# Kernel optimization log

Measured on AMD Instinct MI355X. Metric: run time of the kernel, lower is better.

## Reference

```python
import jax, jax.numpy as jnp
import numpy as np

T, B = 32, 512          # frames, batch
HALF = 42               # rows per hand (21 landmarks x 2 coords)
HF = 300                # per-hand feature size
HID = 500               # hidden size
OUT = 10                # output classes
DN = ('NCH', 'OIH', 'NCH')


def setup_inputs() -> dict:
    key = jax.random.key(0)
    ks = jax.random.split(key, 18)
    n = lambda k, s: jax.random.normal(k, s, dtype=jnp.float32) * 0.05
    return dict(
        hand_data=jax.random.normal(ks[0], (T, B, 2 * HALF), dtype=jnp.float32),
        hidden=jnp.zeros((B, HID), jnp.float32),
        l_conv_w=n(ks[1], (16, 2, 2)), l_conv_b=n(ks[2], (16,)),
        l_fc_w=n(ks[3], (HF, 304)),    l_fc_b=n(ks[4], (HF,)),
        r_conv_w=n(ks[5], (16, 2, 2)), r_conv_b=n(ks[6], (16,)),
        r_fc_w=n(ks[7], (HF, 304)),    r_fc_b=n(ks[8], (HF,)),
        conv2_w=n(ks[9], (32, 2, 2)),  conv2_b=n(ks[10], (32,)),
        l2_w=n(ks[11], (HID, 9504)),   l2_b=n(ks[12], (HID,)),
        h2h_w=n(ks[13], (HID, HID)),   h2h_b=n(ks[14], (HID,)),
        out_w=n(ks[15], (OUT, HID)),   out_b=n(ks[16], (OUT,)),
    )


def _maxpool1d(y, k):
    return jax.lax.reduce_window(y, -jnp.inf, jax.lax.max,
                                 (1, 1, k), (1, 1, 1), 'VALID')


def _hand(x, cw, cb, fw, fb):
    # x: (N, 2, 21) -> conv k2 -> (N,16,20) -> relu -> pool k2 -> (N,16,19)
    y = jax.lax.conv_general_dilated(x, cw, (1,), 'VALID', dimension_numbers=DN)
    y = jax.nn.relu(y + cb[None, :, None])
    y = _maxpool1d(y, 2)
    y = y.reshape(y.shape[0], -1)          # (N, 304)
    return jax.nn.relu(y @ fw.T + fb)      # (N, 300)


def reference(hand_data, hidden,
              l_conv_w, l_conv_b, l_fc_w, l_fc_b,
              r_conv_w, r_conv_b, r_fc_w, r_fc_b,
              conv2_w, conv2_b, l2_w, l2_b,
              h2h_w, h2h_b, out_w, out_b):
    t, b, r = hand_data.shape
    half = r // 2
    # (T,B,42) -> (T*B,21,2) -> (T*B,2,21); per-frame branches have no
    # recurrence, so we vectorize them over all frames at once.
    left = jnp.swapaxes(hand_data[:, :, :half].reshape(t * b, -1, 2), 1, 2)
    right = jnp.swapaxes(hand_data[:, :, half:].reshape(t * b, -1, 2), 1, 2)
    lo = _hand(left, l_conv_w, l_conv_b, l_fc_w, l_fc_b)    # (T*B, 300)
    ro = _hand(right, r_conv_w, r_conv_b, r_fc_w, r_fc_b)   # (T*B, 300)
    both = jnp.stack([lo, ro], axis=1)                       # (T*B, 2, 300)
    y = jax.lax.conv_general_dilated(both, conv2_w, (1,), 'VALID',
                                     dimension_numbers=DN)   # (T*B, 32, 299)
    y = jax.nn.relu(y + conv2_b[None, :, None])
    y = _maxpool1d(y, 3)                                     # (T*B, 32, 297)
    y = y.reshape(t * b, -1)                                 # (T*B, 9504)
    i2h = (y @ l2_w.T + l2_b).reshape(t, b, -1)              # (T, B, 500)

    def step(h, i2h_t):
        h = h @ h2h_w.T + h2h_b                              # hidden = h2h(hidden)
        out = jax.nn.relu((i2h_t + h) @ out_w.T + out_b)
        return h, out

    hidden, outs = jax.lax.scan(step, hidden, i2h)
    return outs[-1], hidden
```

## Files before the change

### kernel.cpp

```cpp
#include <hip/hip_runtime.h>
#include <hip/hip_bf16.h>


typedef __attribute__((ext_vector_type(8))) unsigned short us8;
typedef __attribute__((ext_vector_type(8))) __bf16 bf8v;
typedef __attribute__((ext_vector_type(4))) float f4v;

static __device__ __forceinline__ unsigned short f2bf(float x) {
    __hip_bfloat16 h = __float2bfloat16(x);
    return *reinterpret_cast<unsigned short*>(&h);
}

static __device__ __forceinline__ void gload16(const void* g, void* s) {
    typedef __attribute__((address_space(1))) const void gv_t;
    typedef __attribute__((address_space(3))) void sv_t;
    __builtin_amdgcn_global_load_lds((gv_t*)g, (sv_t*)s, 16, 0, 0);
}

static __device__ __forceinline__ float4 ldg4_guard(
    const float* __restrict__ p, int r, int R, int c, int C, int ld)
{
    float4 v = make_float4(0.f, 0.f, 0.f, 0.f);
    if (r < R) {
        if (c + 3 < C) {
            v = *(const float4*)(p + (size_t)r * ld + c);
        } else {
            float tmp[4] = {0.f, 0.f, 0.f, 0.f};
            for (int u = 0; u < 4; ++u)
                if (c + u < C) tmp[u] = p[(size_t)r * ld + c + u];
            v = make_float4(tmp[0], tmp[1], tmp[2], tmp[3]);
        }
    }
    return v;
}

#define KSTR 9536

__global__ __launch_bounds__(256, 2) void mfma_bt(
    const unsigned short* __restrict__ A, const unsigned short* __restrict__ B,
    float* __restrict__ Cp, int nper, int ntot)
{
    __shared__ alignas(16) unsigned short Al[2][4096];
    __shared__ alignas(16) unsigned short Bl[2][4096];
    const int lid = blockIdx.x;
    const int z = lid & 7;
    const int bm = ((lid >> 3) & 7) * 64, bn = (lid >> 6) * 64;
    int s0 = z * nper;
    int s1 = s0 + nper; if (s1 > ntot) s1 = ntot;
    const int ns = s1 - s0;
    const int t = threadIdx.x, w = t >> 6, l = t & 63;
    const int srow = l >> 3;
    const int sslot = (l & 7) ^ srow;
    const int wm = (w >> 1) * 32, wn = (w & 1) * 32;
    const int fr = l & 15, jj = l >> 4;
    f4v acc[2][2] = {};

    const unsigned short* Ab = A + (size_t)(bm + 16 * w + srow) * KSTR + sslot * 8;
    const unsigned short* Bb = B + (size_t)(bn + 16 * w + srow) * KSTR + sslot * 8;

#define STAGE(buf, st)                                                          \
    {                                                                           \
        size_t k0 = (size_t)(s0 + (st)) * 64;                                   \
        _Pragma("unroll")                                                       \
        for (int q = 0; q < 2; ++q) {                                           \
            gload16(Ab + (size_t)(8 * q) * KSTR + k0,                           \
                    &Al[buf][(16 * w + 8 * q) * 64]);                           \
            gload16(Bb + (size_t)(8 * q) * KSTR + k0,                           \
                    &Bl[buf][(16 * w + 8 * q) * 64]);                           \
        }                                                                       \
    }

#define COMPUTE(buf)                                                            \
    {                                                                           \
        _Pragma("unroll")                                                       \
        for (int kk = 0; kk < 2; ++kk) {                                        \
            bf8v af[2], bf[2];                                                  \
            _Pragma("unroll")                                                   \
            for (int f = 0; f < 2; ++f) {                                       \
                int rA = wm + f * 16 + fr;                                      \
                int pA = (jj + 4 * kk) ^ (rA & 7);                              \
                af[f] = __builtin_bit_cast(bf8v,                                \
                        *(const us8*)&Al[buf][rA * 64 + pA * 8]);               \
                int rB = wn + f * 16 + fr;                                      \
                int pB = (jj + 4 * kk) ^ (rB & 7);                              \
                bf[f] = __builtin_bit_cast(bf8v,                                \
                        *(const us8*)&Bl[buf][rB * 64 + pB * 8]);               \
            }                                                                   \
            _Pragma("unroll")                                                   \
            for (int fi = 0; fi < 2; ++fi)                                      \
                _Pragma("unroll")                                               \
                for (int fj = 0; fj < 2; ++fj)                                  \
                    acc[fi][fj] = __builtin_amdgcn_mfma_f32_16x16x32_bf16(      \
                        af[fi], bf[fj], acc[fi][fj], 0, 0, 0);                  \
        }                                                                       \
    }

    STAGE(0, 0);
    __syncthreads();
    int cur = 0;
    for (int st = 0; st < ns; ++st) {
        if (st + 1 < ns) STAGE(cur ^ 1, st + 1);
        COMPUTE(cur);
        __syncthreads();
        cur ^= 1;
    }

    float* Cz = Cp + (size_t)z * 262144;
#pragma unroll
    for (int fi = 0; fi < 2; ++fi)
#pragma unroll
        for (int fj = 0; fj < 2; ++fj)
#pragma unroll
            for (int r = 0; r < 4; ++r) {
                int m = bm + wm + fi * 16 + jj * 4 + r;
                int n = bn + wn + fj * 16 + fr;
                Cz[(size_t)m * 512 + n] = acc[fi][fj][r];
            }
#undef STAGE
#undef COMPUTE
}


__global__ __launch_bounds__(256) void fc_gemm(
    const float* __restrict__ hpL, const float* __restrict__ hpR,
    const float* __restrict__ lfw, const float* __restrict__ rfw,
    const float* __restrict__ lfb, const float* __restrict__ rfb,
    float* __restrict__ both)
{
    __shared__ alignas(16) float As[16][68];
    __shared__ alignas(16) float Bs[16][68];
    const int hand = blockIdx.z;
    const float* A = hand ? hpR : hpL;
    const float* B = hand ? rfw : lfw;
    const float* bias = hand ? rfb : lfb;
    const int t = threadIdx.x;
    const int bm = blockIdx.x * 64, bn = blockIdx.y * 64;
    const int lr = t >> 2, kq = (t & 3) * 4;
    const int ty = t >> 4, tx = t & 15;
    float acc[4][4] = {};
    float4 a0 = *(const float4*)(A + (size_t)(bm + lr) * 304 + kq);
    float4 b0 = (bn + lr < 300)
        ? *(const float4*)(B + (size_t)(bn + lr) * 304 + kq)
        : make_float4(0.f, 0.f, 0.f, 0.f);
    for (int ks = 0; ks < 19; ++ks) {
        __syncthreads();
        As[kq + 0][lr] = a0.x; As[kq + 1][lr] = a0.y;
        As[kq + 2][lr] = a0.z; As[kq + 3][lr] = a0.w;
        Bs[kq + 0][lr] = b0.x; Bs[kq + 1][lr] = b0.y;
        Bs[kq + 2][lr] = b0.z; Bs[kq + 3][lr] = b0.w;
        __syncthreads();
        if (ks < 18) {
            int kb = (ks + 1) * 16 + kq;
            a0 = *(const float4*)(A + (size_t)(bm + lr) * 304 + kb);
            b0 = (bn + lr < 300)
                ? *(const float4*)(B + (size_t)(bn + lr) * 304 + kb)
                : make_float4(0.f, 0.f, 0.f, 0.f);
        }
#pragma unroll
        for (int k = 0; k < 16; ++k) {
            float4 av = *(const float4*)&As[k][ty * 4];
            float4 bv = *(const float4*)&Bs[k][tx * 4];
            float aa[4] = {av.x, av.y, av.z, av.w};
            float bb[4] = {bv.x, bv.y, bv.z, bv.w};
#pragma unroll
            for (int i = 0; i < 4; ++i)
#pragma unroll
                for (int j = 0; j < 4; ++j)
                    acc[i][j] = fmaf(aa[i], bb[j], acc[i][j]);
        }
    }
#pragma unroll
    for (int i = 0; i < 4; ++i) {
        int m = bm + ty * 4 + i;
#pragma unroll
        for (int j = 0; j < 4; ++j) {
            int n = bn + tx * 4 + j;
            if (n < 300)
                both[(size_t)m * 600 + hand * 300 + n] =
                    fmaxf(acc[i][j] + bias[n], 0.f);
        }
    }
}

__global__ __launch_bounds__(256) void sq_gemm(
    const float* __restrict__ P, float* __restrict__ Psum)
{
    __shared__ alignas(16) float As[16][68];
    __shared__ alignas(16) float Bs[16][68];
    const int t = threadIdx.x;
    const int bm = blockIdx.x * 64, bn = blockIdx.y * 64, z = blockIdx.z;
    const int k0 = z * 128;
    const int kend = (k0 + 128 < 500) ? k0 + 128 : 500;
    const int lr = t >> 2, kq = (t & 3) * 4;
    const int kr = t >> 4, cq = (t & 15) * 4;
    const int ty = t >> 4, tx = t & 15;
    float acc[4][4] = {};
    float4 a0 = ldg4_guard(P, bm + lr, 500, k0 + kq, kend, 500);
    float4 b0 = ldg4_guard(P, k0 + kr, kend, bn + cq, 500, 500);
    for (int ks = 0; ks < 8; ++ks) {
        __syncthreads();
        As[kq + 0][lr] = a0.x; As[kq + 1][lr] = a0.y;
        As[kq + 2][lr] = a0.z; As[kq + 3][lr] = a0.w;
        *(float4*)&Bs[kr][cq] = b0;
        __syncthreads();
        if (ks < 7) {
            a0 = ldg4_guard(P, bm + lr, 500, k0 + (ks + 1) * 16 + kq, kend, 500);
            b0 = ldg4_guard(P, k0 + (ks + 1) * 16 + kr, kend, bn + cq, 500, 500);
        }
#pragma unroll
        for (int k = 0; k < 16; ++k) {
            float4 av = *(const float4*)&As[k][ty * 4];
            float4 bv = *(const float4*)&Bs[k][tx * 4];
            float aa[4] = {av.x, av.y, av.z, av.w};
            float bb[4] = {bv.x, bv.y, bv.z, bv.w};
#pragma unroll
            for (int i = 0; i < 4; ++i)
#pragma unroll
                for (int j = 0; j < 4; ++j)
                    acc[i][j] = fmaf(aa[i], bb[j], acc[i][j]);
        }
    }
    float* Cz = Psum + (size_t)z * 250000;
#pragma unroll
    for (int i = 0; i < 4; ++i) {
        int m = bm + ty * 4 + i;
        if (m >= 500) continue;
#pragma unroll
        for (int j = 0; j < 4; ++j) {
            int n = bn + tx * 4 + j;
            if (n < 500) Cz[(size_t)m * 500 + n] = acc[i][j];
        }
    }
}

__global__ __launch_bounds__(256) void sq_red(
    const float* __restrict__ Psum, float* __restrict__ Pn,
    const float* __restrict__ u, const float* __restrict__ Pold,
    float* __restrict__ un)
{
    __shared__ float red[4];
    const int x = blockIdx.x, t = threadIdx.x;
    if (x < 977) {
        int idx = x * 256 + t;
        if (idx < 250000)
            Pn[idx] = Psum[idx] + Psum[250000 + idx] +
                      Psum[500000 + idx] + Psum[750000 + idx];
    } else {
        int j = x - 977;
        const float* row = Pold + (size_t)j * 500;
        float s = 0.f;
        for (int a = t; a < 500; a += 256) s += u[a] * row[a];
        for (int off = 32; off; off >>= 1) s += __shfl_down(s, off);
        if ((t & 63) == 0) red[t >> 6] = s;
        __syncthreads();
        if (t == 0) un[j] = red[0] + red[1] + red[2] + red[3] + u[j];
    }
}

__global__ __launch_bounds__(256) void h_gemm(
    const float* __restrict__ A, const float* __restrict__ B,
    float* __restrict__ Hsum)
{
    __shared__ alignas(16) float As[16][68];
    __shared__ alignas(16) float Bs[16][68];
    const int t = threadIdx.x;
    const int bm = blockIdx.x * 64, bn = blockIdx.y * 64, z = blockIdx.z;
    const int k0 = z * 128;
    const int kend = (k0 + 128 < 500) ? k0 + 128 : 500;
    const int lr = t >> 2, kq = (t & 3) * 4;
    const int ty = t >> 4, tx = t & 15;
    float acc[4][4] = {};
    float4 a0 = ldg4_guard(A, bm + lr, 512, k0 + kq, kend, 500);
    float4 b0 = ldg4_guard(B, bn + lr, 500, k0 + kq, kend, 500);
    for (int ks = 0; ks < 8; ++ks) {
        __syncthreads();
        As[kq + 0][lr] = a0.x; As[kq + 1][lr] = a0.y;
        As[kq + 2][lr] = a0.z; As[kq + 3][lr] = a0.w;
        Bs[kq + 0][lr] = b0.x; Bs[kq + 1][lr] = b0.y;
        Bs[kq + 2][lr] = b0.z; Bs[kq + 3][lr] = b0.w;
        __syncthreads();
        if (ks < 7) {
            a0 = ldg4_guard(A, bm + lr, 512, k0 + (ks + 1) * 16 + kq, kend, 500);
            b0 = ldg4_guard(B, bn + lr, 500, k0 + (ks + 1) * 16 + kq, kend, 500);
        }
#pragma unroll
        for (int k = 0; k < 16; ++k) {
            float4 av = *(const float4*)&As[k][ty * 4];
            float4 bv = *(const float4*)&Bs[k][tx * 4];
            float aa[4] = {av.x, av.y, av.z, av.w};
            float bb[4] = {bv.x, bv.y, bv.z, bv.w};
#pragma unroll
            for (int i = 0; i < 4; ++i)
#pragma unroll
                for (int j = 0; j < 4; ++j)
                    acc[i][j] = fmaf(aa[i], bb[j], acc[i][j]);
        }
    }
    float* Cz = Hsum + (size_t)z * 256000;
#pragma unroll
    for (int i = 0; i < 4; ++i) {
        int m = bm + ty * 4 + i;
#pragma unroll
        for (int j = 0; j < 4; ++j) {
            int n = bn + tx * 4 + j;
            if (n < 500) Cz[(size_t)m * 500 + n] = acc[i][j];
        }
    }
}

__global__ __launch_bounds__(128) void hand_conv(
    const float* __restrict__ hand,
    const float* __restrict__ lcw, const float* __restrict__ lcb,
    const float* __restrict__ rcw, const float* __restrict__ rcb,
    float* __restrict__ hpL, float* __restrict__ hpR)
{
    const int b = blockIdx.x;
    __shared__ float x[84];
    __shared__ float cw[2][64];
    __shared__ float cb[2][16];
    const int t = threadIdx.x;
    if (t < 84) x[t] = hand[(size_t)b * 84 + t];
    if (t < 64) { cw[0][t] = lcw[t]; cw[1][t] = rcw[t]; }
    if (t < 16) { cb[0][t] = lcb[t]; cb[1][t] = rcb[t]; }
    __syncthreads();
    for (int idx = t; idx < 608; idx += 128) {
        int hi = idx / 304, rem = idx % 304;
        int o = rem / 19, p = rem % 19;
        int off = hi * 42;
        const float* w = cw[hi];
        float w00 = w[o * 4], w01 = w[o * 4 + 1], w10 = w[o * 4 + 2], w11 = w[o * 4 + 3];
        float bs = cb[hi][o];
        float c0 = w00 * x[off + 2 * p] + w01 * x[off + 2 * p + 2] +
                   w10 * x[off + 2 * p + 1] + w11 * x[off + 2 * p + 3] + bs;
        float c1 = w00 * x[off + 2 * p + 2] + w01 * x[off + 2 * p + 4] +
                   w10 * x[off + 2 * p + 3] + w11 * x[off + 2 * p + 5] + bs;
        float v = fmaxf(fmaxf(c0, c1), 0.f);
        (hi ? hpR : hpL)[(size_t)b * 304 + rem] = v;
    }
}

__global__ __launch_bounds__(256) void conv2_feat(
    const float* __restrict__ both, const float* __restrict__ w2g,
    const float* __restrict__ b2g, unsigned short* __restrict__ feat)
{
    const int b = blockIdx.x, t = threadIdx.x;
    __shared__ float s[600];
    __shared__ float w2[128];
    __shared__ float b2[32];
    for (int i = t; i < 600; i += 256) s[i] = both[(size_t)b * 600 + i];
    if (t < 128) w2[t] = w2g[t];
    if (t < 32) b2[t] = b2g[t];
    __syncthreads();
    for (int idx = t; idx < 9536; idx += 256) {
        unsigned short ov = 0;
        if (idx < 9504) {
            int o = idx / 297, p = idx - o * 297;
            float w0 = w2[o * 4], w1 = w2[o * 4 + 1];
            float w2v = w2[o * 4 + 2], w3 = w2[o * 4 + 3], bb = b2[o];
            float m = -1e30f;
#pragma unroll
            for (int q = 0; q < 3; ++q) {
                float c = w0 * s[p + q] + w1 * s[p + q + 1] +
                          w2v * s[300 + p + q] + w3 * s[301 + p + q] + bb;
                m = fmaxf(m, c);
            }
            ov = f2bf(fmaxf(m, 0.f));
        }
        feat[(size_t)b * 9536 + idx] = ov;
    }
}

__global__ __launch_bounds__(256) void cvt_w(
    const float* __restrict__ W, unsigned short* __restrict__ Wb)
{
    int idx = blockIdx.x * 256 + threadIdx.x;
    int row = idx / 1192;
    int k8 = (idx - row * 1192) * 8;
    if (row >= 512) return;
    us8 o = (us8)0;
    if (row < 500 && k8 < 9504) {
        const float* p = W + (size_t)row * 9504 + k8;
        float4 v0 = *(const float4*)p;
        float4 v1 = *(const float4*)(p + 4);
        o[0] = f2bf(v0.x); o[1] = f2bf(v0.y); o[2] = f2bf(v0.z); o[3] = f2bf(v0.w);
        o[4] = f2bf(v1.x); o[5] = f2bf(v1.y); o[6] = f2bf(v1.z); o[7] = f2bf(v1.w);
    }
    *(us8*)(Wb + (size_t)row * 9536 + k8) = o;
}

__global__ __launch_bounds__(256) void out_final(
    const float* __restrict__ Cp, const float* __restrict__ l2b,
    const float* __restrict__ Hsum, const float* __restrict__ u32,
    const float* __restrict__ ow, const float* __restrict__ ob,
    float* __restrict__ out, float* __restrict__ hout)
{
    const int b = blockIdx.x, t = threadIdx.x;
    __shared__ float sj[512];
    __shared__ float red[10][4];
    for (int j = t; j < 500; j += 256) {
        float ih = l2b[j];
#pragma unroll
        for (int zz = 0; zz < 8; ++zz)
            ih += Cp[(size_t)zz * 262144 + (size_t)b * 512 + j];
        float h = u32[j];
#pragma unroll
        for (int zz = 0; zz < 4; ++zz)
            h += Hsum[(size_t)zz * 256000 + (size_t)b * 500 + j];
        hout[(size_t)b * 500 + j] = h;
        sj[j] = ih + h;
    }
    __syncthreads();
    const int w = t >> 6;
    for (int o = 0; o < 10; ++o) {
        float acc = 0.f;
        if (t < 500) acc += sj[t] * ow[o * 500 + t];
        if (t + 256 < 500) acc += sj[t + 256] * ow[o * 500 + t + 256];
        for (int off = 32; off; off >>= 1) acc += __shfl_down(acc, off);
        if ((t & 63) == 0) red[o][w] = acc;
    }
    __syncthreads();
    if (t < 10)
        out[(size_t)b * 10 + t] =
            fmaxf(red[t][0] + red[t][1] + red[t][2] + red[t][3] + ob[t], 0.f);
}

extern "C" void kernel_launch(void* const* d_in, const int* in_sizes, int n_in,
                              void* d_out, int out_size, void* d_ws, size_t ws_size,
                              hipStream_t stream) {
    const float* hand   = (const float*)d_in[0];
    const float* hidden = (const float*)d_in[1];
    const float* lcw = (const float*)d_in[2];
    const float* lcb = (const float*)d_in[3];
    const float* lfw = (const float*)d_in[4];
    const float* lfb = (const float*)d_in[5];
    const float* rcw = (const float*)d_in[6];
    const float* rcb = (const float*)d_in[7];
    const float* rfw = (const float*)d_in[8];
    const float* rfb = (const float*)d_in[9];
    const float* w2  = (const float*)d_in[10];
    const float* b2  = (const float*)d_in[11];
    const float* l2w = (const float*)d_in[12];
    const float* l2b = (const float*)d_in[13];
    const float* hw  = (const float*)d_in[14];
    const float* hb  = (const float*)d_in[15];
    const float* ow  = (const float*)d_in[16];
    const float* ob  = (const float*)d_in[17];

    char* wsb = (char*)d_ws;
    float* Cp   = (float*)wsb;
    float* hpL  = (float*)wsb;
    float* hpR  = (float*)(wsb + 622592);
    float* both = (float*)(wsb + 1245184);
    char* base1 = wsb + 8388608;
    unsigned short* featb = (unsigned short*)base1;
    unsigned short* wbf   = (unsigned short*)(base1 + 9764864);
    float* Psum = (float*)base1;
    float* Pa   = (float*)(base1 + 4000000);
    float* Pb   = (float*)(base1 + 5000000);
    float* ua   = (float*)(base1 + 6000000);
    float* ub   = (float*)(base1 + 6002000);
    float* Hsum = (float*)(base1 + 9764864);

    float* out  = (float*)d_out;
    float* hout = out + 5120;

    cvt_w<<<2384, 256, 0, stream>>>(l2w, wbf);
    hand_conv<<<512, 128, 0, stream>>>(hand + (size_t)31 * 512 * 84,
                                       lcw, lcb, rcw, rcb, hpL, hpR);
    fc_gemm<<<dim3(8, 5, 2), 256, 0, stream>>>(hpL, hpR, lfw, rfw, lfb, rfb, both);
    conv2_feat<<<512, 256, 0, stream>>>(both, w2, b2, featb);
    mfma_bt<<<512, 256, 0, stream>>>(featb, wbf, Cp, 19, 149);

    const float* Pcur = hw;
    const float* ucur = hb;
    float* Pn[5] = {Pa, Pb, Pa, Pb, Pa};
    float* un[5] = {ua, ub, ua, ub, ua};
    for (int i = 0; i < 5; i++) {
        sq_gemm<<<dim3(8, 8, 4), 256, 0, stream>>>(Pcur, Psum);
        sq_red<<<1477, 256, 0, stream>>>(Psum, Pn[i], ucur, Pcur, un[i]);
        Pcur = Pn[i];
        ucur = un[i];
    }
    h_gemm<<<dim3(8, 8, 4), 256, 0, stream>>>(hidden, Pcur, Hsum);
    out_final<<<512, 256, 0, stream>>>(Cp, l2b, Hsum, ucur, ow, ob, out, hout);
}
```

Measured before the change: 149.6 us.

## Square h2h matrix with split-bf16 MFMA kernel fused with bias recurrence

Replaces the FP32 split-K SIMT squaring GEMM plus its reduction kernel with a single MFMA kernel. It uses a hi/lo bf16 decomposition (three MFMAs per tile) to keep near-fp32 accuracy. The kernel writes both row-major and transposed split copies of the result for the next squaring, and folds the bias-vector update into extra blocks of the same launch. This halves the launch count in the repeated-squaring chain and moves the math onto matrix cores, at the cost of extra split/transposed stores and some loss of precision from dropping the lo*lo term.

```diff
diff --git a/kernel.cpp b/kernel.cpp
--- a/kernel.cpp
+++ b/kernel.cpp
@@ -9,6 +9,15 @@
 static __device__ __forceinline__ unsigned short f2bf(float x) {
     __hip_bfloat16 h = __float2bfloat16(x);
     return *reinterpret_cast<unsigned short*>(&h);
+}
+static __device__ __forceinline__ float bf2f(unsigned short u) {
+    __hip_bfloat16 h = *reinterpret_cast<__hip_bfloat16*>(&u);
+    return __bfloat162float(h);
+}
+static __device__ __forceinline__ void splitf(float f, unsigned short& h,
+                                              unsigned short& l) {
+    h = f2bf(f);
+    l = f2bf(f - bf2f(h));
 }
 
 static __device__ __forceinline__ void gload16(const void* g, void* s) {
@@ -120,6 +129,149 @@
 #undef COMPUTE
 }
 
+__global__ __launch_bounds__(256) void prep_pw(
+    const float* __restrict__ P,
+    unsigned short* __restrict__ hiR, unsigned short* __restrict__ loR,
+    unsigned short* __restrict__ hiC, unsigned short* __restrict__ loC)
+{
+    __shared__ unsigned short shH[64][65];
+    __shared__ unsigned short shL[64][65];
+    const int bm = (blockIdx.x & 7) * 64, bn = (blockIdx.x >> 3) * 64;
+    const int t = threadIdx.x;
+    for (int idx = t; idx < 4096; idx += 256) {
+        int m = idx >> 6, n = idx & 63;
+        int gm = bm + m, gn = bn + n;
+        float f = (gm < 500 && gn < 500) ? P[(size_t)gm * 500 + gn] : 0.f;
+        unsigned short h, l;
+        splitf(f, h, l);
+        hiR[(size_t)gm * 512 + gn] = h;
+        loR[(size_t)gm * 512 + gn] = l;
+        shH[m][n] = h; shL[m][n] = l;
+    }
+    __syncthreads();
+    for (int idx = t; idx < 4096; idx += 256) {
+        int nn = idx >> 6, mm = idx & 63;
+        hiC[(size_t)(bn + nn) * 512 + bm + mm] = shH[mm][nn];
+        loC[(size_t)(bn + nn) * 512 + bm + mm] = shL[mm][nn];
+    }
+}
+
+__global__ __launch_bounds__(256, 2) void sq_mfma(
+    const unsigned short* __restrict__ hiR, const unsigned short* __restrict__ loR,
+    const unsigned short* __restrict__ hiC, const unsigned short* __restrict__ loC,
+    float* __restrict__ dstF,
+    unsigned short* __restrict__ dhiR, unsigned short* __restrict__ dloR,
+    unsigned short* __restrict__ dhiC, unsigned short* __restrict__ dloC,
+    const float* __restrict__ vsrc, const float* __restrict__ u_in,
+    float* __restrict__ u_out)
+{
+    __shared__ alignas(16) unsigned short AhiL[2][4096];
+    __shared__ alignas(16) unsigned short AloL[2][4096];
+    __shared__ alignas(16) unsigned short BhiL[2][4096];
+    __shared__ alignas(16) unsigned short BloL[2][4096];
+    const int lid = blockIdx.x, t = threadIdx.x;
+    if (lid >= 64) {
+        const int j = lid - 64;
+        float* red = (float*)AhiL;
+        float s = 0.f;
+        for (int a = t; a < 500; a += 256)
+            s += u_in[a] * vsrc[(size_t)j * 500 + a];
+        for (int off = 32; off; off >>= 1) s += __shfl_down(s, off);
+        if ((t & 63) == 0) red[t >> 6] = s;
+        __syncthreads();
+        if (t == 0) u_out[j] = red[0] + red[1] + red[2] + red[3] + u_in[j];
+        return;
+    }
+    const int bm = (lid & 7) * 64, bn = (lid >> 3) * 64;
+    const int w = t >> 6, l = t & 63;
+    const int srow = l >> 3;
+    const int sslot = (l & 7) ^ srow;
+    const int wm = (w >> 1) * 32, wn = (w & 1) * 32;
+    const int fr = l & 15, jj = l >> 4;
+    f4v acc[2][2] = {};
+
+    const size_t offA = (size_t)(bm + 16 * w + srow) * 512 + sslot * 8;
+    const size_t offB = (size_t)(bn + 16 * w + srow) * 512 + sslot * 8;
+
+#define SQSTAGE(buf, st)                                                        \
+    {                                                                           \
+        size_t k0 = (size_t)(st) * 64;                                          \
+        _Pragma("unroll")                                                       \
+        for (int q = 0; q < 2; ++q) {                                           \
+            size_t sa = offA + (size_t)(8 * q) * 512 + k0;                      \
+            size_t sb = offB + (size_t)(8 * q) * 512 + k0;                      \
+            gload16(hiR + sa, &AhiL[buf][(16 * w + 8 * q) * 64]);               \
+            gload16(loR + sa, &AloL[buf][(16 * w + 8 * q) * 64]);               \
+            gload16(hiC + sb, &BhiL[buf][(16 * w + 8 * q) * 64]);               \
+            gload16(loC + sb, &BloL[buf][(16 * w + 8 * q) * 64]);               \
+        }                                                                       \
+    }
+#define SQCOMPUTE(buf)                                                          \
+    {                                                                           \
+        _Pragma("unroll")                                                       \
+        for (int kk = 0; kk < 2; ++kk) {                                        \
+            bf8v ah[2], al[2], bh[2], bl[2];                                    \
+            _Pragma("unroll")                                                   \
+            for (int f = 0; f < 2; ++f) {                                       \
+                int rA = wm + f * 16 + fr;                                      \
+                int pA = (jj + 4 * kk) ^ (rA & 7);                              \
+                ah[f] = __builtin_bit_cast(bf8v,                                \
+                        *(const us8*)&AhiL[buf][rA * 64 + pA * 8]);             \
+                al[f] = __builtin_bit_cast(bf8v,                                \
+                        *(const us8*)&AloL[buf][rA * 64 + pA * 8]);             \
+                int rB = wn + f * 16 + fr;                                      \
+                int pB = (jj + 4 * kk) ^ (rB & 7);                              \
+                bh[f] = __builtin_bit_cast(bf8v,                                \
+                        *(const us8*)&BhiL[buf][rB * 64 + pB * 8]);             \
+                bl[f] = __builtin_bit_cast(bf8v,                                \
+                        *(const us8*)&BloL[buf][rB * 64 + pB * 8]);             \
+            }                                                                   \
+            _Pragma("unroll")                                                   \
+            for (int fi = 0; fi < 2; ++fi)                                      \
+                _Pragma("unroll")                                               \
+                for (int fj = 0; fj < 2; ++fj) {                                \
+                    acc[fi][fj] = __builtin_amdgcn_mfma_f32_16x16x32_bf16(      \
+                        ah[fi], bh[fj], acc[fi][fj], 0, 0, 0);                  \
+                    acc[fi][fj] = __builtin_amdgcn_mfma_f32_16x16x32_bf16(      \
+                        ah[fi], bl[fj], acc[fi][fj], 0, 0, 0);                  \
+                    acc[fi][fj] = __builtin_amdgcn_mfma_f32_16x16x32_bf16(      \
+                        al[fi], bh[fj], acc[fi][fj], 0, 0, 0);                  \
+                }                                                               \
+        }                                                                       \
+    }
+
+    SQSTAGE(0, 0);
+    __syncthreads();
+    int cur = 0;
+    for (int st = 0; st < 8; ++st) {
+        if (st + 1 < 8) SQSTAGE(cur ^ 1, st + 1);
+        SQCOMPUTE(cur);
+        __syncthreads();
+        cur ^= 1;
+    }
+
+#pragma unroll
+    for (int fi = 0; fi < 2; ++fi)
+#pragma unroll
+        for (int fj = 0; fj < 2; ++fj)
+#pragma unroll
+            for (int r = 0; r < 4; ++r) {
+                int m = bm + wm + fi * 16 + jj * 4 + r;
+                int n = bn + wn + fj * 16 + fr;
+                float v = acc[fi][fj][r];
+                if (m < 500 && n < 500) dstF[(size_t)m * 500 + n] = v;
+                if (dhiR) {
+                    unsigned short h, lo2;
+                    splitf(v, h, lo2);
+                    dhiR[(size_t)m * 512 + n] = h;
+                    dloR[(size_t)m * 512 + n] = lo2;
+                    dhiC[(size_t)n * 512 + m] = h;
+                    dloC[(size_t)n * 512 + m] = lo2;
+                }
+            }
+#undef SQSTAGE
+#undef SQCOMPUTE
+}
 
 __global__ __launch_bounds__(256) void fc_gemm(
     const float* __restrict__ hpL, const float* __restrict__ hpR,
@@ -179,81 +331,6 @@
                 both[(size_t)m * 600 + hand * 300 + n] =
                     fmaxf(acc[i][j] + bias[n], 0.f);
         }
-    }
-}
-
-__global__ __launch_bounds__(256) void sq_gemm(
-    const float* __restrict__ P, float* __restrict__ Psum)
-{
-    __shared__ alignas(16) float As[16][68];
-    __shared__ alignas(16) float Bs[16][68];
-    const int t = threadIdx.x;
-    const int bm = blockIdx.x * 64, bn = blockIdx.y * 64, z = blockIdx.z;
-    const int k0 = z * 128;
-    const int kend = (k0 + 128 < 500) ? k0 + 128 : 500;
-    const int lr = t >> 2, kq = (t & 3) * 4;
-    const int kr = t >> 4, cq = (t & 15) * 4;
-    const int ty = t >> 4, tx = t & 15;
-    float acc[4][4] = {};
-    float4 a0 = ldg4_guard(P, bm + lr, 500, k0 + kq, kend, 500);
-    float4 b0 = ldg4_guard(P, k0 + kr, kend, bn + cq, 500, 500);
-    for (int ks = 0; ks < 8; ++ks) {
-        __syncthreads();
-        As[kq + 0][lr] = a0.x; As[kq + 1][lr] = a0.y;
-        As[kq + 2][lr] = a0.z; As[kq + 3][lr] = a0.w;
-        *(float4*)&Bs[kr][cq] = b0;
-        __syncthreads();
-        if (ks < 7) {
-            a0 = ldg4_guard(P, bm + lr, 500, k0 + (ks + 1) * 16 + kq, kend, 500);
-            b0 = ldg4_guard(P, k0 + (ks + 1) * 16 + kr, kend, bn + cq, 500, 500);
-        }
-#pragma unroll
-        for (int k = 0; k < 16; ++k) {
-            float4 av = *(const float4*)&As[k][ty * 4];
-            float4 bv = *(const float4*)&Bs[k][tx * 4];
-            float aa[4] = {av.x, av.y, av.z, av.w};
-            float bb[4] = {bv.x, bv.y, bv.z, bv.w};
-#pragma unroll
-            for (int i = 0; i < 4; ++i)
-#pragma unroll
-                for (int j = 0; j < 4; ++j)
-                    acc[i][j] = fmaf(aa[i], bb[j], acc[i][j]);
-        }
-    }
-    float* Cz = Psum + (size_t)z * 250000;
-#pragma unroll
-    for (int i = 0; i < 4; ++i) {
-        int m = bm + ty * 4 + i;
-        if (m >= 500) continue;
-#pragma unroll
-        for (int j = 0; j < 4; ++j) {
-            int n = bn + tx * 4 + j;
-            if (n < 500) Cz[(size_t)m * 500 + n] = acc[i][j];
-        }
-    }
-}
-
-__global__ __launch_bounds__(256) void sq_red(
-    const float* __restrict__ Psum, float* __restrict__ Pn,
-    const float* __restrict__ u, const float* __restrict__ Pold,
-    float* __restrict__ un)
-{
-    __shared__ float red[4];
-    const int x = blockIdx.x, t = threadIdx.x;
-    if (x < 977) {
-        int idx = x * 256 + t;
-        if (idx < 250000)
-            Pn[idx] = Psum[idx] + Psum[250000 + idx] +
-                      Psum[500000 + idx] + Psum[750000 + idx];
-    } else {
-        int j = x - 977;
-        const float* row = Pold + (size_t)j * 500;
-        float s = 0.f;
-        for (int a = t; a < 500; a += 256) s += u[a] * row[a];
-        for (int off = 32; off; off >>= 1) s += __shfl_down(s, off);
-        if ((t & 63) == 0) red[t >> 6] = s;
-        __syncthreads();
-        if (t == 0) un[j] = red[0] + red[1] + red[2] + red[3] + u[j];
     }
 }
 
@@ -454,11 +531,18 @@
     char* base1 = wsb + 8388608;
     unsigned short* featb = (unsigned short*)base1;
     unsigned short* wbf   = (unsigned short*)(base1 + 9764864);
-    float* Psum = (float*)base1;
-    float* Pa   = (float*)(base1 + 4000000);
-    float* Pb   = (float*)(base1 + 5000000);
-    float* ua   = (float*)(base1 + 6000000);
-    float* ub   = (float*)(base1 + 6002000);
+    float* Pa = (float*)base1;
+    float* Pb = (float*)(base1 + 1000000);
+    float* ua = (float*)(base1 + 2000000);
+    float* ub = (float*)(base1 + 2002048);
+    unsigned short* hiRA = (unsigned short*)(base1 + 2004096);
+    unsigned short* loRA = hiRA + 262144;
+    unsigned short* hiCA = loRA + 262144;
+    unsigned short* loCA = hiCA + 262144;
+    unsigned short* hiRB = loCA + 262144;
+    unsigned short* loRB = hiRB + 262144;
+    unsigned short* hiCB = loRB + 262144;
+    unsigned short* loCB = hiCB + 262144;
     float* Hsum = (float*)(base1 + 9764864);
 
     float* out  = (float*)d_out;
@@ -471,16 +555,19 @@
     conv2_feat<<<512, 256, 0, stream>>>(both, w2, b2, featb);
     mfma_bt<<<512, 256, 0, stream>>>(featb, wbf, Cp, 19, 149);
 
-    const float* Pcur = hw;
-    const float* ucur = hb;
-    float* Pn[5] = {Pa, Pb, Pa, Pb, Pa};
-    float* un[5] = {ua, ub, ua, ub, ua};
-    for (int i = 0; i < 5; i++) {
-        sq_gemm<<<dim3(8, 8, 4), 256, 0, stream>>>(Pcur, Psum);
-        sq_red<<<1477, 256, 0, stream>>>(Psum, Pn[i], ucur, Pcur, un[i]);
-        Pcur = Pn[i];
-        ucur = un[i];
-    }
-    h_gemm<<<dim3(8, 8, 4), 256, 0, stream>>>(hidden, Pcur, Hsum);
-    out_final<<<512, 256, 0, stream>>>(Cp, l2b, Hsum, ucur, ow, ob, out, hout);
-}
+    prep_pw<<<64, 256, 0, stream>>>(hw, hiRA, loRA, hiCA, loCA);
+    sq_mfma<<<564, 256, 0, stream>>>(hiRA, loRA, hiCA, loCA, Pa,
+                                     hiRB, loRB, hiCB, loCB, hw, hb, ua);
+    sq_mfma<<<564, 256, 0, stream>>>(hiRB, loRB, hiCB, loCB, Pb,
+                                     hiRA, loRA, hiCA, loCA, Pa, ua, ub);
+    sq_mfma<<<564, 256, 0, stream>>>(hiRA, loRA, hiCA, loCA, Pa,
+                                     hiRB, loRB, hiCB, loCB, Pb, ub, ua);
+    sq_mfma<<<564, 256, 0, stream>>>(hiRB, loRB, hiCB, loCB, Pb,
+                                     hiRA, loRA, hiCA, loCA, Pa, ua, ub);
+    sq_mfma<<<564, 256, 0, stream>>>(hiRA, loRA, hiCA, loCA, Pa,
+                                     nullptr, nullptr, nullptr, nullptr,
+                                     Pb, ub, ua);
+
+    h_gemm<<<dim3(8, 8, 4), 256, 0, stream>>>(hidden, Pa, Hsum);
+    out_final<<<512, 256, 0, stream>>>(Cp, l2b, Hsum, ua, ow, ob, out, hout);
+}
```

After: 157.1 us. 1.05x slower.

## Fuse split-K reduction into consumer loads by storing interleaved partial sums

Applied to the files above, without the earlier changes.

The separate split-K reduction kernel for each matrix-squaring step is removed. Each squaring GEMM now writes its four K-slice partials interleaved as a float4 per element, and the next GEMM (and the final hidden GEMM) sums those four values while loading. The bias-vector update u' = P·u + u is folded into extra blocks of the same launch, which halves the launch count in the power chain. In exchange, every consumer load reads four times as many bytes and does the adds, and writes are strided by four.

```diff
diff --git a/kernel.cpp b/kernel.cpp
--- a/kernel.cpp
+++ b/kernel.cpp
@@ -32,6 +32,25 @@
         }
     }
     return v;
+}
+
+static __device__ __forceinline__ float4 ld4_zsum(
+    const float* __restrict__ p, int r, int R, int c, int C)
+{
+    float4 o = make_float4(0.f, 0.f, 0.f, 0.f);
+    if (r < R) {
+        const float4* q = (const float4*)p + (size_t)r * 500 + c;
+        float vv[4] = {0.f, 0.f, 0.f, 0.f};
+#pragma unroll
+        for (int u = 0; u < 4; ++u) {
+            if (c + u < C) {
+                float4 v = q[u];
+                vv[u] = (v.x + v.y) + (v.z + v.w);
+            }
+        }
+        o = make_float4(vv[0], vv[1], vv[2], vv[3]);
+    }
+    return o;
 }
 
 #define KSTR 9536
@@ -120,6 +139,135 @@
 #undef COMPUTE
 }
 
+__global__ __launch_bounds__(256) void sq_int(
+    const float* __restrict__ src, int imode, float* __restrict__ dstI,
+    const float* __restrict__ u_in, float* __restrict__ u_out)
+{
+    __shared__ alignas(16) float As[16][68];
+    __shared__ alignas(16) float Bs[16][68];
+    const int lid = blockIdx.x, t = threadIdx.x;
+    if (lid >= 256) {
+        const int j = lid - 256;
+        float* red = (float*)As;
+        float s = 0.f;
+        if (imode) {
+            const float4* q = (const float4*)src + (size_t)j * 500;
+            for (int a = t; a < 500; a += 256) {
+                float4 v = q[a];
+                s += u_in[a] * ((v.x + v.y) + (v.z + v.w));
+            }
+        } else {
+            for (int a = t; a < 500; a += 256)
+                s += u_in[a] * src[(size_t)j * 500 + a];
+        }
+        for (int off = 32; off; off >>= 1) s += __shfl_down(s, off);
+        if ((t & 63) == 0) red[t >> 6] = s;
+        __syncthreads();
+        if (t == 0) u_out[j] = red[0] + red[1] + red[2] + red[3] + u_in[j];
+        return;
+    }
+    const int z = lid & 3;
+    const int bm = ((lid >> 2) & 7) * 64, bn = ((lid >> 5) & 7) * 64;
+    const int k0 = z * 128;
+    const int kend = (k0 + 128 < 500) ? k0 + 128 : 500;
+    const int lr = t >> 2, kq = (t & 3) * 4;
+    const int kr = t >> 4, cq = (t & 15) * 4;
+    const int ty = t >> 4, tx = t & 15;
+    float acc[4][4] = {};
+    float4 a0 = imode ? ld4_zsum(src, bm + lr, 500, k0 + kq, kend)
+                      : ldg4_guard(src, bm + lr, 500, k0 + kq, kend, 500);
+    float4 b0 = imode ? ld4_zsum(src, k0 + kr, kend, bn + cq, 500)
+                      : ldg4_guard(src, k0 + kr, kend, bn + cq, 500, 500);
+    for (int ks = 0; ks < 8; ++ks) {
+        __syncthreads();
+        As[kq + 0][lr] = a0.x; As[kq + 1][lr] = a0.y;
+        As[kq + 2][lr] = a0.z; As[kq + 3][lr] = a0.w;
+        *(float4*)&Bs[kr][cq] = b0;
+        __syncthreads();
+        if (ks < 7) {
+            int ka = k0 + (ks + 1) * 16;
+            a0 = imode ? ld4_zsum(src, bm + lr, 500, ka + kq, kend)
+                       : ldg4_guard(src, bm + lr, 500, ka + kq, kend, 500);
+            b0 = imode ? ld4_zsum(src, ka + kr, kend, bn + cq, 500)
+                       : ldg4_guard(src, ka + kr, kend, bn + cq, 500, 500);
+        }
+#pragma unroll
+        for (int k = 0; k < 16; ++k) {
+            float4 av = *(const float4*)&As[k][ty * 4];
+            float4 bv = *(const float4*)&Bs[k][tx * 4];
+            float aa[4] = {av.x, av.y, av.z, av.w};
+            float bb[4] = {bv.x, bv.y, bv.z, bv.w};
+#pragma unroll
+            for (int i = 0; i < 4; ++i)
+#pragma unroll
+                for (int j = 0; j < 4; ++j)
+                    acc[i][j] = fmaf(aa[i], bb[j], acc[i][j]);
+        }
+    }
+#pragma unroll
+    for (int i = 0; i < 4; ++i) {
+        int m = bm + ty * 4 + i;
+        if (m >= 500) continue;
+#pragma unroll
+        for (int j = 0; j < 4; ++j) {
+            int n = bn + tx * 4 + j;
+            if (n < 500)
+                dstI[((size_t)m * 500 + n) * 4 + z] = acc[i][j];
+        }
+    }
+}
+
+__global__ __launch_bounds__(256) void h_gemm_int(
+    const float* __restrict__ A, const float* __restrict__ BI,
+    float* __restrict__ Hsum)
+{
+    __shared__ alignas(16) float As[16][68];
+    __shared__ alignas(16) float Bs[16][68];
+    const int t = threadIdx.x;
+    const int bm = blockIdx.x * 64, bn = blockIdx.y * 64, z = blockIdx.z;
+    const int k0 = z * 128;
+    const int kend = (k0 + 128 < 500) ? k0 + 128 : 500;
+    const int lr = t >> 2, kq = (t & 3) * 4;
+    const int ty = t >> 4, tx = t & 15;
+    float acc[4][4] = {};
+    float4 a0 = ldg4_guard(A, bm + lr, 512, k0 + kq, kend, 500);
+    float4 b0 = ld4_zsum(BI, bn + lr, 500, k0 + kq, kend);
+    for (int ks = 0; ks < 8; ++ks) {
+        __syncthreads();
+        As[kq + 0][lr] = a0.x; As[kq + 1][lr] = a0.y;
+        As[kq + 2][lr] = a0.z; As[kq + 3][lr] = a0.w;
+        Bs[kq + 0][lr] = b0.x; Bs[kq + 1][lr] = b0.y;
+        Bs[kq + 2][lr] = b0.z; Bs[kq + 3][lr] = b0.w;
+        __syncthreads();
+        if (ks < 7) {
+            int ka = k0 + (ks + 1) * 16;
+            a0 = ldg4_guard(A, bm + lr, 512, ka + kq, kend, 500);
+            b0 = ld4_zsum(BI, bn + lr, 500, ka + kq, kend);
+        }
+#pragma unroll
+        for (int k = 0; k < 16; ++k) {
+            float4 av = *(const float4*)&As[k][ty * 4];
+            float4 bv = *(const float4*)&Bs[k][tx * 4];
+            float aa[4] = {av.x, av.y, av.z, av.w};
+            float bb[4] = {bv.x, bv.y, bv.z, bv.w};
+#pragma unroll
+            for (int i = 0; i < 4; ++i)
+#pragma unroll
+                for (int j = 0; j < 4; ++j)
+                    acc[i][j] = fmaf(aa[i], bb[j], acc[i][j]);
+        }
+    }
+    float* Cz = Hsum + (size_t)z * 256000;
+#pragma unroll
+    for (int i = 0; i < 4; ++i) {
+        int m = bm + ty * 4 + i;
+#pragma unroll
+        for (int j = 0; j < 4; ++j) {
+            int n = bn + tx * 4 + j;
+            if (n < 500) Cz[(size_t)m * 500 + n] = acc[i][j];
+        }
+    }
+}
 
 __global__ __launch_bounds__(256) void fc_gemm(
     const float* __restrict__ hpL, const float* __restrict__ hpR,
@@ -178,132 +326,6 @@
             if (n < 300)
                 both[(size_t)m * 600 + hand * 300 + n] =
                     fmaxf(acc[i][j] + bias[n], 0.f);
-        }
-    }
-}
-
-__global__ __launch_bounds__(256) void sq_gemm(
-    const float* __restrict__ P, float* __restrict__ Psum)
-{
-    __shared__ alignas(16) float As[16][68];
-    __shared__ alignas(16) float Bs[16][68];
-    const int t = threadIdx.x;
-    const int bm = blockIdx.x * 64, bn = blockIdx.y * 64, z = blockIdx.z;
-    const int k0 = z * 128;
-    const int kend = (k0 + 128 < 500) ? k0 + 128 : 500;
-    const int lr = t >> 2, kq = (t & 3) * 4;
-    const int kr = t >> 4, cq = (t & 15) * 4;
-    const int ty = t >> 4, tx = t & 15;
-    float acc[4][4] = {};
-    float4 a0 = ldg4_guard(P, bm + lr, 500, k0 + kq, kend, 500);
-    float4 b0 = ldg4_guard(P, k0 + kr, kend, bn + cq, 500, 500);
-    for (int ks = 0; ks < 8; ++ks) {
-        __syncthreads();
-        As[kq + 0][lr] = a0.x; As[kq + 1][lr] = a0.y;
-        As[kq + 2][lr] = a0.z; As[kq + 3][lr] = a0.w;
-        *(float4*)&Bs[kr][cq] = b0;
-        __syncthreads();
-        if (ks < 7) {
-            a0 = ldg4_guard(P, bm + lr, 500, k0 + (ks + 1) * 16 + kq, kend, 500);
-            b0 = ldg4_guard(P, k0 + (ks + 1) * 16 + kr, kend, bn + cq, 500, 500);
-        }
-#pragma unroll
-        for (int k = 0; k < 16; ++k) {
-            float4 av = *(const float4*)&As[k][ty * 4];
-            float4 bv = *(const float4*)&Bs[k][tx * 4];
-            float aa[4] = {av.x, av.y, av.z, av.w};
-            float bb[4] = {bv.x, bv.y, bv.z, bv.w};
-#pragma unroll
-            for (int i = 0; i < 4; ++i)
-#pragma unroll
-                for (int j = 0; j < 4; ++j)
-                    acc[i][j] = fmaf(aa[i], bb[j], acc[i][j]);
-        }
-    }
-    float* Cz = Psum + (size_t)z * 250000;
-#pragma unroll
-    for (int i = 0; i < 4; ++i) {
-        int m = bm + ty * 4 + i;
-        if (m >= 500) continue;
-#pragma unroll
-        for (int j = 0; j < 4; ++j) {
-            int n = bn + tx * 4 + j;
-            if (n < 500) Cz[(size_t)m * 500 + n] = acc[i][j];
-        }
-    }
-}
-
-__global__ __launch_bounds__(256) void sq_red(
-    const float* __restrict__ Psum, float* __restrict__ Pn,
-    const float* __restrict__ u, const float* __restrict__ Pold,
-    float* __restrict__ un)
-{
-    __shared__ float red[4];
-    const int x = blockIdx.x, t = threadIdx.x;
-    if (x < 977) {
-        int idx = x * 256 + t;
-        if (idx < 250000)
-            Pn[idx] = Psum[idx] + Psum[250000 + idx] +
-                      Psum[500000 + idx] + Psum[750000 + idx];
-    } else {
-        int j = x - 977;
-        const float* row = Pold + (size_t)j * 500;
-        float s = 0.f;
-        for (int a = t; a < 500; a += 256) s += u[a] * row[a];
-        for (int off = 32; off; off >>= 1) s += __shfl_down(s, off);
-        if ((t & 63) == 0) red[t >> 6] = s;
-        __syncthreads();
-        if (t == 0) un[j] = red[0] + red[1] + red[2] + red[3] + u[j];
-    }
-}
-
-__global__ __launch_bounds__(256) void h_gemm(
-    const float* __restrict__ A, const float* __restrict__ B,
-    float* __restrict__ Hsum)
-{
-    __shared__ alignas(16) float As[16][68];
-    __shared__ alignas(16) float Bs[16][68];
-    const int t = threadIdx.x;
-    const int bm = blockIdx.x * 64, bn = blockIdx.y * 64, z = blockIdx.z;
-    const int k0 = z * 128;
-    const int kend = (k0 + 128 < 500) ? k0 + 128 : 500;
-    const int lr = t >> 2, kq = (t & 3) * 4;
-    const int ty = t >> 4, tx = t & 15;
-    float acc[4][4] = {};
-    float4 a0 = ldg4_guard(A, bm + lr, 512, k0 + kq, kend, 500);
-    float4 b0 = ldg4_guard(B, bn + lr, 500, k0 + kq, kend, 500);
-    for (int ks = 0; ks < 8; ++ks) {
-        __syncthreads();
-        As[kq + 0][lr] = a0.x; As[kq + 1][lr] = a0.y;
-        As[kq + 2][lr] = a0.z; As[kq + 3][lr] = a0.w;
-        Bs[kq + 0][lr] = b0.x; Bs[kq + 1][lr] = b0.y;
-        Bs[kq + 2][lr] = b0.z; Bs[kq + 3][lr] = b0.w;
-        __syncthreads();
-        if (ks < 7) {
-            a0 = ldg4_guard(A, bm + lr, 512, k0 + (ks + 1) * 16 + kq, kend, 500);
-            b0 = ldg4_guard(B, bn + lr, 500, k0 + (ks + 1) * 16 + kq, kend, 500);
-        }
-#pragma unroll
-        for (int k = 0; k < 16; ++k) {
-            float4 av = *(const float4*)&As[k][ty * 4];
-            float4 bv = *(const float4*)&Bs[k][tx * 4];
-            float aa[4] = {av.x, av.y, av.z, av.w};
-            float bb[4] = {bv.x, bv.y, bv.z, bv.w};
-#pragma unroll
-            for (int i = 0; i < 4; ++i)
-#pragma unroll
-                for (int j = 0; j < 4; ++j)
-                    acc[i][j] = fmaf(aa[i], bb[j], acc[i][j]);
-        }
-    }
-    float* Cz = Hsum + (size_t)z * 256000;
-#pragma unroll
-    for (int i = 0; i < 4; ++i) {
-        int m = bm + ty * 4 + i;
-#pragma unroll
-        for (int j = 0; j < 4; ++j) {
-            int n = bn + tx * 4 + j;
-            if (n < 500) Cz[(size_t)m * 500 + n] = acc[i][j];
         }
     }
 }
@@ -454,11 +476,10 @@
     char* base1 = wsb + 8388608;
     unsigned short* featb = (unsigned short*)base1;
     unsigned short* wbf   = (unsigned short*)(base1 + 9764864);
-    float* Psum = (float*)base1;
-    float* Pa   = (float*)(base1 + 4000000);
-    float* Pb   = (float*)(base1 + 5000000);
-    float* ua   = (float*)(base1 + 6000000);
-    float* ub   = (float*)(base1 + 6002000);
+    float* Ia = (float*)base1;
+    float* Ib = (float*)(base1 + 4000000);
+    float* ua = (float*)(base1 + 8000000);
+    float* ub = (float*)(base1 + 8002048);
     float* Hsum = (float*)(base1 + 9764864);
 
     float* out  = (float*)d_out;
@@ -471,16 +492,12 @@
     conv2_feat<<<512, 256, 0, stream>>>(both, w2, b2, featb);
     mfma_bt<<<512, 256, 0, stream>>>(featb, wbf, Cp, 19, 149);
 
-    const float* Pcur = hw;
-    const float* ucur = hb;
-    float* Pn[5] = {Pa, Pb, Pa, Pb, Pa};
-    float* un[5] = {ua, ub, ua, ub, ua};
-    for (int i = 0; i < 5; i++) {
-        sq_gemm<<<dim3(8, 8, 4), 256, 0, stream>>>(Pcur, Psum);
-        sq_red<<<1477, 256, 0, stream>>>(Psum, Pn[i], ucur, Pcur, un[i]);
-        Pcur = Pn[i];
-        ucur = un[i];
-    }
-    h_gemm<<<dim3(8, 8, 4), 256, 0, stream>>>(hidden, Pcur, Hsum);
-    out_final<<<512, 256, 0, stream>>>(Cp, l2b, Hsum, ucur, ow, ob, out, hout);
-}
+    sq_int<<<756, 256, 0, stream>>>(hw, 0, Ia, hb, ua);
+    sq_int<<<756, 256, 0, stream>>>(Ia, 1, Ib, ua, ub);
+    sq_int<<<756, 256, 0, stream>>>(Ib, 1, Ia, ub, ua);
+    sq_int<<<756, 256, 0, stream>>>(Ia, 1, Ib, ua, ub);
+    sq_int<<<756, 256, 0, stream>>>(Ib, 1, Ia, ub, ua);
+
+    h_gemm_int<<<dim3(8, 8, 4), 256, 0, stream>>>(hidden, Ia, Hsum);
+    out_final<<<512, 256, 0, stream>>>(Cp, l2b, Hsum, ua, ow, ob, out, hout);
+}
```

Result: slower. 198.5 us (+32.7%).

## Fuse weight bf16 conversion into MFMA GEMM and hand conv into FC GEMM

Applied to the files above, without the earlier changes.

Removes the separate cvt_w kernel by loading fp32 l2 weights directly in the MFMA GEMM and converting them to bf16 in registers before writing LDS. Also removes the hand_conv kernel by computing the conv+relu+pool features on the fly inside the FC GEMM from a shared-memory tile of the input frame. This drops two launches and the intermediate global round-trips, but each GEMM block now rereads and reconverts fp32 weights (8 z-splits times 8 bm tiles), which doubles weight bytes per load, and the FC kernel recomputes the conv values for every column tile.

```diff
diff --git a/kernel.cpp b/kernel.cpp
--- a/kernel.cpp
+++ b/kernel.cpp
@@ -36,8 +36,8 @@
 
 #define KSTR 9536
 
-__global__ __launch_bounds__(256, 2) void mfma_bt(
-    const unsigned short* __restrict__ A, const unsigned short* __restrict__ B,
+__global__ __launch_bounds__(256, 2) void mfma_fw(
+    const unsigned short* __restrict__ A, const float* __restrict__ Wf,
     float* __restrict__ Cp, int nper, int ntot)
 {
     __shared__ alignas(16) unsigned short Al[2][4096];
@@ -54,22 +54,45 @@
     const int wm = (w >> 1) * 32, wn = (w & 1) * 32;
     const int fr = l & 15, jj = l >> 4;
     f4v acc[2][2] = {};
+    float4 vb0[2], vb1[2];
 
     const unsigned short* Ab = A + (size_t)(bm + 16 * w + srow) * KSTR + sslot * 8;
-    const unsigned short* Bb = B + (size_t)(bn + 16 * w + srow) * KSTR + sslot * 8;
-
-#define STAGE(buf, st)                                                          \
+
+#define ALOAD(buf, st)                                                          \
     {                                                                           \
         size_t k0 = (size_t)(s0 + (st)) * 64;                                   \
         _Pragma("unroll")                                                       \
-        for (int q = 0; q < 2; ++q) {                                           \
+        for (int q = 0; q < 2; ++q)                                             \
             gload16(Ab + (size_t)(8 * q) * KSTR + k0,                           \
                     &Al[buf][(16 * w + 8 * q) * 64]);                           \
-            gload16(Bb + (size_t)(8 * q) * KSTR + k0,                           \
-                    &Bl[buf][(16 * w + 8 * q) * 64]);                           \
+    }
+#define BLOAD(st)                                                               \
+    {                                                                           \
+        size_t kb = (size_t)(s0 + (st)) * 64 + sslot * 8;                       \
+        _Pragma("unroll")                                                       \
+        for (int q = 0; q < 2; ++q) {                                           \
+            int r = bn + 16 * w + 8 * q + srow;                                 \
+            vb0[q] = make_float4(0.f, 0.f, 0.f, 0.f);                           \
+            vb1[q] = vb0[q];                                                    \
+            if (r < 500 && kb < 9504) {                                         \
+                const float* p = Wf + (size_t)r * 9504 + kb;                    \
+                vb0[q] = *(const float4*)p;                                     \
+                vb1[q] = *(const float4*)(p + 4);                               \
+            }                                                                   \
         }                                                                       \
     }
-
+#define BWRITE(buf)                                                             \
+    {                                                                           \
+        _Pragma("unroll")                                                       \
+        for (int q = 0; q < 2; ++q) {                                           \
+            us8 ov;                                                             \
+            ov[0] = f2bf(vb0[q].x); ov[1] = f2bf(vb0[q].y);                     \
+            ov[2] = f2bf(vb0[q].z); ov[3] = f2bf(vb0[q].w);                     \
+            ov[4] = f2bf(vb1[q].x); ov[5] = f2bf(vb1[q].y);                     \
+            ov[6] = f2bf(vb1[q].z); ov[7] = f2bf(vb1[q].w);                     \
+            *(us8*)&Bl[buf][(16 * w + 8 * q + srow) * 64 + (l & 7) * 8] = ov;   \
+        }                                                                       \
+    }
 #define COMPUTE(buf)                                                            \
     {                                                                           \
         _Pragma("unroll")                                                       \
@@ -95,12 +118,18 @@
         }                                                                       \
     }
 
-    STAGE(0, 0);
+    BLOAD(0);
+    ALOAD(0, 0);
+    BWRITE(0);
     __syncthreads();
     int cur = 0;
     for (int st = 0; st < ns; ++st) {
-        if (st + 1 < ns) STAGE(cur ^ 1, st + 1);
+        if (st + 1 < ns) {
+            BLOAD(st + 1);
+            ALOAD(cur ^ 1, st + 1);
+        }
         COMPUTE(cur);
+        if (st + 1 < ns) BWRITE(cur ^ 1);
         __syncthreads();
         cur ^= 1;
     }
@@ -116,29 +145,58 @@
                 int n = bn + wn + fj * 16 + fr;
                 Cz[(size_t)m * 512 + n] = acc[fi][fj][r];
             }
-#undef STAGE
+#undef ALOAD
+#undef BLOAD
+#undef BWRITE
 #undef COMPUTE
 }
 
-
-__global__ __launch_bounds__(256) void fc_gemm(
-    const float* __restrict__ hpL, const float* __restrict__ hpR,
+__global__ __launch_bounds__(256) void fc_fused(
+    const float* __restrict__ hand31,
     const float* __restrict__ lfw, const float* __restrict__ rfw,
     const float* __restrict__ lfb, const float* __restrict__ rfb,
+    const float* __restrict__ lcw, const float* __restrict__ lcb,
+    const float* __restrict__ rcw, const float* __restrict__ rcb,
     float* __restrict__ both)
 {
     __shared__ alignas(16) float As[16][68];
     __shared__ alignas(16) float Bs[16][68];
+    __shared__ alignas(16) float xs[64][84];
+    __shared__ float cw[64];
+    __shared__ float cb[16];
     const int hand = blockIdx.z;
-    const float* A = hand ? hpR : hpL;
     const float* B = hand ? rfw : lfw;
     const float* bias = hand ? rfb : lfb;
     const int t = threadIdx.x;
     const int bm = blockIdx.x * 64, bn = blockIdx.y * 64;
+    const int off = hand * 42;
+    if (t < 64) cw[t] = hand ? rcw[t] : lcw[t];
+    if (t < 16) cb[t] = hand ? rcb[t] : lcb[t];
+    for (int idx = t; idx < 64 * 21; idx += 256) {
+        int r = idx / 21, c = idx % 21;
+        *(float4*)&xs[r][c * 4] =
+            *(const float4*)(hand31 + (size_t)(bm + r) * 84 + c * 4);
+    }
+    __syncthreads();
     const int lr = t >> 2, kq = (t & 3) * 4;
     const int ty = t >> 4, tx = t & 15;
     float acc[4][4] = {};
-    float4 a0 = *(const float4*)(A + (size_t)(bm + lr) * 304 + kq);
+
+    auto hpval = [&](int k) -> float {
+        unsigned o = (unsigned)k / 19u;
+        int p = k - (int)o * 19;
+        float w00 = cw[o * 4], w01 = cw[o * 4 + 1];
+        float w10 = cw[o * 4 + 2], w11 = cw[o * 4 + 3];
+        float bs = cb[o];
+        const float* x = &xs[lr][off + 2 * p];
+        float c0 = w00 * x[0] + w01 * x[2] + w10 * x[1] + w11 * x[3] + bs;
+        float c1 = w00 * x[2] + w01 * x[4] + w10 * x[3] + w11 * x[5] + bs;
+        return fmaxf(fmaxf(c0, c1), 0.f);
+    };
+
+    float4 a0;
+    a0.x = hpval(kq + 0); a0.y = hpval(kq + 1);
+    a0.z = hpval(kq + 2); a0.w = hpval(kq + 3);
     float4 b0 = (bn + lr < 300)
         ? *(const float4*)(B + (size_t)(bn + lr) * 304 + kq)
         : make_float4(0.f, 0.f, 0.f, 0.f);
@@ -151,7 +209,8 @@
         __syncthreads();
         if (ks < 18) {
             int kb = (ks + 1) * 16 + kq;
-            a0 = *(const float4*)(A + (size_t)(bm + lr) * 304 + kb);
+            a0.x = hpval(kb + 0); a0.y = hpval(kb + 1);
+            a0.z = hpval(kb + 2); a0.w = hpval(kb + 3);
             b0 = (bn + lr < 300)
                 ? *(const float4*)(B + (size_t)(bn + lr) * 304 + kb)
                 : make_float4(0.f, 0.f, 0.f, 0.f);
@@ -305,37 +364,6 @@
             int n = bn + tx * 4 + j;
             if (n < 500) Cz[(size_t)m * 500 + n] = acc[i][j];
         }
-    }
-}
-
-__global__ __launch_bounds__(128) void hand_conv(
-    const float* __restrict__ hand,
-    const float* __restrict__ lcw, const float* __restrict__ lcb,
-    const float* __restrict__ rcw, const float* __restrict__ rcb,
-    float* __restrict__ hpL, float* __restrict__ hpR)
-{
-    const int b = blockIdx.x;
-    __shared__ float x[84];
-    __shared__ float cw[2][64];
-    __shared__ float cb[2][16];
-    const int t = threadIdx.x;
-    if (t < 84) x[t] = hand[(size_t)b * 84 + t];
-    if (t < 64) { cw[0][t] = lcw[t]; cw[1][t] = rcw[t]; }
-    if (t < 16) { cb[0][t] = lcb[t]; cb[1][t] = rcb[t]; }
-    __syncthreads();
-    for (int idx = t; idx < 608; idx += 128) {
-        int hi = idx / 304, rem = idx % 304;
-        int o = rem / 19, p = rem % 19;
-        int off = hi * 42;
-        const float* w = cw[hi];
-        float w00 = w[o * 4], w01 = w[o * 4 + 1], w10 = w[o * 4 + 2], w11 = w[o * 4 + 3];
-        float bs = cb[hi][o];
-        float c0 = w00 * x[off + 2 * p] + w01 * x[off + 2 * p + 2] +
-                   w10 * x[off + 2 * p + 1] + w11 * x[off + 2 * p + 3] + bs;
-        float c1 = w00 * x[off + 2 * p + 2] + w01 * x[off + 2 * p + 4] +
-                   w10 * x[off + 2 * p + 3] + w11 * x[off + 2 * p + 5] + bs;
-        float v = fmaxf(fmaxf(c0, c1), 0.f);
-        (hi ? hpR : hpL)[(size_t)b * 304 + rem] = v;
     }
 }
 
@@ -368,24 +396,6 @@
         }
         feat[(size_t)b * 9536 + idx] = ov;
     }
-}
-
-__global__ __launch_bounds__(256) void cvt_w(
-    const float* __restrict__ W, unsigned short* __restrict__ Wb)
-{
-    int idx = blockIdx.x * 256 + threadIdx.x;
-    int row = idx / 1192;
-    int k8 = (idx - row * 1192) * 8;
-    if (row >= 512) return;
-    us8 o = (us8)0;
-    if (row < 500 && k8 < 9504) {
-        const float* p = W + (size_t)row * 9504 + k8;
-        float4 v0 = *(const float4*)p;
-        float4 v1 = *(const float4*)(p + 4);
-        o[0] = f2bf(v0.x); o[1] = f2bf(v0.y); o[2] = f2bf(v0.z); o[3] = f2bf(v0.w);
-        o[4] = f2bf(v1.x); o[5] = f2bf(v1.y); o[6] = f2bf(v1.z); o[7] = f2bf(v1.w);
-    }
-    *(us8*)(Wb + (size_t)row * 9536 + k8) = o;
 }
 
 __global__ __launch_bounds__(256) void out_final(
@@ -448,12 +458,9 @@
 
     char* wsb = (char*)d_ws;
     float* Cp   = (float*)wsb;
-    float* hpL  = (float*)wsb;
-    float* hpR  = (float*)(wsb + 622592);
-    float* both = (float*)(wsb + 1245184);
+    float* both = (float*)wsb;
     char* base1 = wsb + 8388608;
     unsigned short* featb = (unsigned short*)base1;
-    unsigned short* wbf   = (unsigned short*)(base1 + 9764864);
     float* Psum = (float*)base1;
     float* Pa   = (float*)(base1 + 4000000);
     float* Pb   = (float*)(base1 + 5000000);
@@ -464,12 +471,12 @@
     float* out  = (float*)d_out;
     float* hout = out + 5120;
 
-    cvt_w<<<2384, 256, 0, stream>>>(l2w, wbf);
-    hand_conv<<<512, 128, 0, stream>>>(hand + (size_t)31 * 512 * 84,
-                                       lcw, lcb, rcw, rcb, hpL, hpR);
-    fc_gemm<<<dim3(8, 5, 2), 256, 0, stream>>>(hpL, hpR, lfw, rfw, lfb, rfb, both);
+    const float* hand31 = hand + (size_t)31 * 512 * 84;
+
+    fc_fused<<<dim3(8, 5, 2), 256, 0, stream>>>(hand31, lfw, rfw, lfb, rfb,
+                                                lcw, lcb, rcw, rcb, both);
     conv2_feat<<<512, 256, 0, stream>>>(both, w2, b2, featb);
-    mfma_bt<<<512, 256, 0, stream>>>(featb, wbf, Cp, 19, 149);
+    mfma_fw<<<512, 256, 0, stream>>>(featb, l2w, Cp, 19, 149);
 
     const float* Pcur = hw;
     const float* ucur = hb;
```

Result: no change. 151.2 us (+1.1%).
